# Performance work log

Measured on AMD Instinct MI355X. Metric: run time of the kernel, lower is better.

## Reference

```python
import jax, jax.numpy as jnp
import numpy as np

TEMPLATE_SZ = 7
MAX_SR = 3


def setup_inputs() -> dict:
    key = jax.random.key(0)
    # image-like values in [0, 255) since the module ends with a uint8 cast
    x = jax.random.uniform(key, (2, 1, 192, 192), dtype=jnp.float32) * 255.0
    return {"inputs": x, "search_range": 3}


def reference(inputs, search_range):
    # Equivalent math to: pad(max_sr) -> unfold(k, pad=k//2) -> unfold(s) ->
    # permute -> slice sub-window -> reshape -> uint8.
    # Both zero-pads commute, so fold them into one pad and gather directly,
    # avoiding the huge duplicated double-im2col intermediate.
    k = TEMPLATE_SZ
    max_sr = MAX_SR
    cv = 2 * search_range + 1          # cost_volume_sz
    offset = max_sr - search_range
    B, C, H, W = inputs.shape          # C == 1 (implied by the torch view)
    pad = max_sr + k // 2              # combined zero padding
    Q = jnp.pad(inputs[:, 0].astype(jnp.float32), ((0, 0), (pad, pad), (pad, pad)))
    r = offset + jnp.arange(cv)        # search offsets within max window
    t = jnp.arange(k)                  # template offsets
    # windows[b,i,j,dy,dx,ty,tx] = Q[b, i + r[dy] + ty, j + r[dx] + tx]
    iy = jnp.arange(H)[:, None, None] + r[None, :, None] + t[None, None, :]  # [H, cv, k]
    jx = jnp.arange(W)[:, None, None] + r[None, :, None] + t[None, None, :]  # [W, cv, k]
    win = Q[:, iy[:, None, :, None, :, None], jx[None, :, None, :, None, :]]  # [B,H,W,cv,cv,k,k]
    return win.reshape(B, H, W, cv * cv, k * k).astype(jnp.uint8)
```

## Files before the change

kernel.cpp:

```cpp
#include <hip/hip_runtime.h>


#define KT 7
#define K2 49
#define MAX_SR 3
#define B_ 2
#define H_ 192
#define W_ 192
#define HW (H_ * W_)
#define PAD 6
#define NT 512
#define RMAX 5
#define PS 17
#define NGROUPS (B_ * H_ * W_ / 4)
#define TABN (4 * NT * RMAX)

typedef int vint4 __attribute__((ext_vector_type(4)));

__device__ __forceinline__ int tab_entry(int jj, int cv, int offset, int d,
                                         int cvmagic) {
    if (jj >= 4 * d) jj = 4 * d - 1;
    int p_in = (jj >= d) + (jj >= 2 * d) + (jj >= 3 * d);
    int j  = jj - p_in * d;
    int rr = j / K2;
    int tt = j - rr * K2;
    int ry = (rr * cvmagic) >> 16;
    int rx = rr - ry * cv;
    int ty = tt / KT;
    int tx = tt - ty * KT;
    return 4 * ((offset + ry + ty) * PS + (offset + rx + tx) + p_in);
}

__global__ __launch_bounds__(256) void tab_kernel(
    int* __restrict__ tab, int cv, int offset, int d, int cvmagic)
{
    int jj = blockIdx.x * 256 + threadIdx.x;
    if (jj < TABN) tab[jj] = tab_entry(jj, cv, offset, d, cvmagic);
}

__global__ __launch_bounds__(NT, 6) void esw_kernel(
    const float* __restrict__ in, int* __restrict__ out,
    const int* __restrict__ tab,
    int cv, int offset, int d, int cvmagic)
{
    __shared__ int patch[13 * PS + 4];

    const int tid = threadIdx.x;
    const int g   = blockIdx.x;

    vint4 f[RMAX];
    if (tab) {
        #pragma unroll
        for (int r = 0; r < RMAX; ++r)
            f[r] = *(const vint4*)(tab + 4 * (tid + NT * r));
    } else {
        #pragma unroll
        for (int r = 0; r < RMAX; ++r) {
            int j4 = 4 * (tid + NT * r);
            #pragma unroll
            for (int u = 0; u < 4; ++u)
                f[r][u] = tab_entry(j4 + u, cv, offset, d, cvmagic);
        }
    }

    const int pix0 = 4 * g;
    const int b   = pix0 / HW;
    const int rem = pix0 - b * HW;
    const int h   = rem / W_;
    const int w   = rem - h * W_;

    if (tid < 13 * 16) {
        int dy = tid >> 4;
        int dx = tid & 15;
        int y = h + dy - PAD;
        int x = w + dx - PAD;
        int v = 0;
        if ((unsigned)y < (unsigned)H_ && (unsigned)x < (unsigned)W_)
            v = (int)in[b * HW + y * W_ + x];
        patch[dy * PS + dx] = v;
    }
    __syncthreads();

    int* op = out + (long long)g * (long long)(4 * d);
    const char* pb = (const char*)patch;
    #pragma unroll
    for (int r = 0; r < RMAX; ++r) {
        int q = tid + NT * r;
        if (q < d) {
            vint4 v;
            v.x = *(const int*)(pb + f[r].x);
            v.y = *(const int*)(pb + f[r].y);
            v.z = *(const int*)(pb + f[r].z);
            v.w = *(const int*)(pb + f[r].w);
            *(vint4*)(op + 4 * q) = v;
        }
    }
}

extern "C" void kernel_launch(void* const* d_in, const int* in_sizes, int n_in,
                              void* d_out, int out_size, void* d_ws, size_t ws_size,
                              hipStream_t stream) {
    const float* in = (const float*)d_in[0];
    int* out = (int*)d_out;

    int cv2 = out_size / (B_ * H_ * W_ * K2);
    int cv = 1;
    while (cv * cv < cv2) ++cv;
    int offset = MAX_SR - (cv - 1) / 2;
    int d = cv2 * K2;
    int cvmagic = 65536 / cv + 1;

    int* tab = (ws_size >= (size_t)(TABN * sizeof(int))) ? (int*)d_ws : nullptr;
    if (tab)
        tab_kernel<<<(TABN + 255) / 256, 256, 0, stream>>>(tab, cv, offset, d,
                                                           cvmagic);
    esw_kernel<<<NGROUPS, NT, 0, stream>>>(in, out, tab, cv, offset, d, cvmagic);
}
```

Baseline: 696.9 us.

## Persistent blocks with double-buffered LDS patch and replicated copies to cut bank conflicts

Result: no change. 710.3 us (+1.9%).

```diff
diff --git a/kernel.cpp b/kernel.cpp
--- a/kernel.cpp
+++ b/kernel.cpp
@@ -12,7 +12,12 @@
 #define NT 512
 #define RMAX 5
 #define PS 17
+#define REP 4
+#define CSTR 232
+#define BUFI (REP * CSTR)
 #define NGROUPS (B_ * H_ * W_ / 4)
+#define NBLOCKS 1024
+#define NITER (NGROUPS / NBLOCKS)
 #define TABN (4 * NT * RMAX)
 
 typedef int vint4 __attribute__((ext_vector_type(4)));
@@ -38,61 +43,101 @@
     if (jj < TABN) tab[jj] = tab_entry(jj, cv, offset, d, cvmagic);
 }
 
-__global__ __launch_bounds__(NT, 6) void esw_kernel(
+__global__ __launch_bounds__(NT, 8) void esw_kernel(
     const float* __restrict__ in, int* __restrict__ out,
     const int* __restrict__ tab,
     int cv, int offset, int d, int cvmagic)
 {
-    __shared__ int patch[13 * PS + 4];
+    __shared__ int patch[2][BUFI + 8];
 
     const int tid = threadIdx.x;
-    const int g   = blockIdx.x;
+    const int bid = blockIdx.x;
+    const int cshift = (tid & 3) * (CSTR * 4);
 
     vint4 f[RMAX];
     if (tab) {
         #pragma unroll
-        for (int r = 0; r < RMAX; ++r)
-            f[r] = *(const vint4*)(tab + 4 * (tid + NT * r));
+        for (int r = 0; r < RMAX; ++r) {
+            vint4 t = *(const vint4*)(tab + 4 * (tid + NT * r));
+            t.x += cshift; t.y += cshift; t.z += cshift; t.w += cshift;
+            f[r] = t;
+        }
     } else {
         #pragma unroll
         for (int r = 0; r < RMAX; ++r) {
             int j4 = 4 * (tid + NT * r);
             #pragma unroll
             for (int u = 0; u < 4; ++u)
-                f[r][u] = tab_entry(j4 + u, cv, offset, d, cvmagic);
+                f[r][u] = tab_entry(j4 + u, cv, offset, d, cvmagic) + cshift;
         }
     }
 
-    const int pix0 = 4 * g;
-    const int b   = pix0 / HW;
-    const int rem = pix0 - b * HW;
-    const int h   = rem / W_;
-    const int w   = rem - h * W_;
+    const int sidx = tid < 13 * 16 ? tid : 13 * 16 - 1;
+    const int sdy = sidx >> 4;
+    const int sdx = sidx & 15;
+    const int swa = sdy * PS + sdx;
 
-    if (tid < 13 * 16) {
-        int dy = tid >> 4;
-        int dx = tid & 15;
-        int y = h + dy - PAD;
-        int x = w + dx - PAD;
+    {
+        const int pix0 = 4 * bid;
+        const int b   = pix0 / HW;
+        const int rem = pix0 - b * HW;
+        const int h   = rem / W_;
+        const int w   = rem - h * W_;
+        int y = h + sdy - PAD;
+        int x = w + sdx - PAD;
         int v = 0;
         if ((unsigned)y < (unsigned)H_ && (unsigned)x < (unsigned)W_)
             v = (int)in[b * HW + y * W_ + x];
-        patch[dy * PS + dx] = v;
+        #pragma unroll
+        for (int c = 0; c < REP; ++c) patch[0][c * CSTR + swa] = v;
     }
-    __syncthreads();
+    asm volatile("s_waitcnt lgkmcnt(0)" ::: "memory");
+    __builtin_amdgcn_sched_barrier(0);
+    __builtin_amdgcn_s_barrier();
+    __builtin_amdgcn_sched_barrier(0);
 
-    int* op = out + (long long)g * (long long)(4 * d);
-    const char* pb = (const char*)patch;
-    #pragma unroll
-    for (int r = 0; r < RMAX; ++r) {
-        int q = tid + NT * r;
-        if (q < d) {
-            vint4 v;
-            v.x = *(const int*)(pb + f[r].x);
-            v.y = *(const int*)(pb + f[r].y);
-            v.z = *(const int*)(pb + f[r].z);
-            v.w = *(const int*)(pb + f[r].w);
-            *(vint4*)(op + 4 * q) = v;
+    int cur = 0;
+    for (int it = 0; it < NITER; ++it) {
+        const int g = it * NBLOCKS + bid;
+        const int have = (it + 1 < NITER);
+
+        int vnext = 0;
+        if (have) {
+            const int pix0 = 4 * (g + NBLOCKS);
+            const int b   = pix0 / HW;
+            const int rem = pix0 - b * HW;
+            const int h   = rem / W_;
+            const int w   = rem - h * W_;
+            int y = h + sdy - PAD;
+            int x = w + sdx - PAD;
+            if ((unsigned)y < (unsigned)H_ && (unsigned)x < (unsigned)W_)
+                vnext = (int)in[b * HW + y * W_ + x];
+        }
+
+        int* op = out + g * (4 * d);
+        const char* pb = (const char*)&patch[cur][0];
+        #pragma unroll
+        for (int r = 0; r < RMAX; ++r) {
+            int q = tid + NT * r;
+            if (q < d) {
+                vint4 v;
+                v.x = *(const int*)(pb + f[r].x);
+                v.y = *(const int*)(pb + f[r].y);
+                v.z = *(const int*)(pb + f[r].z);
+                v.w = *(const int*)(pb + f[r].w);
+                *(vint4*)(op + 4 * q) = v;
+            }
+        }
+
+        if (have) {
+            int* pn = &patch[cur ^ 1][0];
+            #pragma unroll
+            for (int c = 0; c < REP; ++c) pn[c * CSTR + swa] = vnext;
+            asm volatile("s_waitcnt lgkmcnt(0)" ::: "memory");
+            __builtin_amdgcn_sched_barrier(0);
+            __builtin_amdgcn_s_barrier();
+            __builtin_amdgcn_sched_barrier(0);
+            cur ^= 1;
         }
     }
 }
@@ -114,5 +159,5 @@
     if (tab)
         tab_kernel<<<(TABN + 255) / 256, 256, 0, stream>>>(tab, cv, offset, d,
                                                            cvmagic);
-    esw_kernel<<<NGROUPS, NT, 0, stream>>>(in, out, tab, cv, offset, d, cvmagic);
+    esw_kernel<<<NBLOCKS, NT, 0, stream>>>(in, out, tab, cv, offset, d, cvmagic);
 }
```

## Use persistent per-wave groups with private LDS patches and swizzled indexing

Applied to the files above, without the earlier changes.

Result: no change. 693.0 us, median of 2 (-0.6%).

```diff
diff --git a/kernel.cpp b/kernel.cpp
--- a/kernel.cpp
+++ b/kernel.cpp
@@ -9,13 +9,19 @@
 #define W_ 192
 #define HW (H_ * W_)
 #define PAD 6
-#define NT 512
-#define RMAX 5
+#define NT 256
+#define NBLOCKS 512
+#define WPB (NT / 64)
+#define NWAVES (NBLOCKS * WPB)
 #define PS 17
+#define BUFI 280
 #define NGROUPS (B_ * H_ * W_ / 4)
-#define TABN (4 * NT * RMAX)
+#define TABQ 2560
+#define TABN (4 * TABQ)
 
 typedef int vint4 __attribute__((ext_vector_type(4)));
+
+__device__ __forceinline__ int swz(int e) { return e + (e >> 2); }
 
 __device__ __forceinline__ int tab_entry(int jj, int cv, int offset, int d,
                                          int cvmagic) {
@@ -28,7 +34,8 @@
     int rx = rr - ry * cv;
     int ty = tt / KT;
     int tx = tt - ty * KT;
-    return 4 * ((offset + ry + ty) * PS + (offset + rx + tx) + p_in);
+    int e = (offset + ry + ty) * PS + (offset + rx + tx) + p_in;
+    return 4 * swz(e);
 }
 
 __global__ __launch_bounds__(256) void tab_kernel(
@@ -38,62 +45,72 @@
     if (jj < TABN) tab[jj] = tab_entry(jj, cv, offset, d, cvmagic);
 }
 
-__global__ __launch_bounds__(NT, 6) void esw_kernel(
+__global__ __launch_bounds__(NT, 2) void esw_kernel(
     const float* __restrict__ in, int* __restrict__ out,
     const int* __restrict__ tab,
     int cv, int offset, int d, int cvmagic)
 {
-    __shared__ int patch[13 * PS + 4];
+    __shared__ int patch[WPB][BUFI];
 
-    const int tid = threadIdx.x;
-    const int g   = blockIdx.x;
+    const int tid  = threadIdx.x;
+    const int lane = tid & 63;
+    const int wv   = tid >> 6;
+    int* const pbuf = patch[wv];
+    const char* const pb = (const char*)pbuf;
 
-    vint4 f[RMAX];
-    if (tab) {
+    const int NR  = (4 * d + 255) >> 8;
+    const int wid = blockIdx.x * WPB + wv;
+
+    for (int g = wid; g < NGROUPS; g += NWAVES) {
+        const int pix0 = 4 * g;
+        const int b   = pix0 / HW;
+        const int rem = pix0 - b * HW;
+        const int h   = rem / W_;
+        const int w   = rem - h * W_;
         #pragma unroll
-        for (int r = 0; r < RMAX; ++r)
-            f[r] = *(const vint4*)(tab + 4 * (tid + NT * r));
-    } else {
-        #pragma unroll
-        for (int r = 0; r < RMAX; ++r) {
-            int j4 = 4 * (tid + NT * r);
-            #pragma unroll
-            for (int u = 0; u < 4; ++u)
-                f[r][u] = tab_entry(j4 + u, cv, offset, d, cvmagic);
+        for (int k = 0; k < 4; ++k) {
+            int e = lane + 64 * k;
+            if (e < 13 * 16) {
+                int dy = e >> 4, dx = e & 15;
+                int y = h + dy - PAD, x = w + dx - PAD;
+                int v = 0;
+                if ((unsigned)y < (unsigned)H_ && (unsigned)x < (unsigned)W_)
+                    v = (int)in[b * HW + y * W_ + x];
+                pbuf[swz(dy * PS + dx)] = v;
+            }
         }
-    }
+        asm volatile("s_waitcnt lgkmcnt(0)" ::: "memory");
 
-    const int pix0 = 4 * g;
-    const int b   = pix0 / HW;
-    const int rem = pix0 - b * HW;
-    const int h   = rem / W_;
-    const int w   = rem - h * W_;
-
-    if (tid < 13 * 16) {
-        int dy = tid >> 4;
-        int dx = tid & 15;
-        int y = h + dy - PAD;
-        int x = w + dx - PAD;
-        int v = 0;
-        if ((unsigned)y < (unsigned)H_ && (unsigned)x < (unsigned)W_)
-            v = (int)in[b * HW + y * W_ + x];
-        patch[dy * PS + dx] = v;
-    }
-    __syncthreads();
-
-    int* op = out + (long long)g * (long long)(4 * d);
-    const char* pb = (const char*)patch;
-    #pragma unroll
-    for (int r = 0; r < RMAX; ++r) {
-        int q = tid + NT * r;
-        if (q < d) {
-            vint4 v;
-            v.x = *(const int*)(pb + f[r].x);
-            v.y = *(const int*)(pb + f[r].y);
-            v.z = *(const int*)(pb + f[r].z);
-            v.w = *(const int*)(pb + f[r].w);
-            *(vint4*)(op + 4 * q) = v;
+        int* op = out + g * (4 * d);
+        if (tab) {
+            vint4 t = *(const vint4*)(tab + 4 * lane);
+            for (int r = 0; r < NR; ++r) {
+                vint4 tn = *(const vint4*)(tab + 4 * (64 * (r + 1) + lane));
+                int q = 64 * r + lane;
+                if (q < d) {
+                    vint4 v;
+                    v.x = *(const int*)(pb + t.x);
+                    v.y = *(const int*)(pb + t.y);
+                    v.z = *(const int*)(pb + t.z);
+                    v.w = *(const int*)(pb + t.w);
+                    *(vint4*)(op + 4 * q) = v;
+                }
+                t = tn;
+            }
+        } else {
+            for (int r = 0; r < NR; ++r) {
+                int q = 64 * r + lane;
+                if (q < d) {
+                    vint4 v;
+                    v.x = *(const int*)(pb + tab_entry(4 * q + 0, cv, offset, d, cvmagic));
+                    v.y = *(const int*)(pb + tab_entry(4 * q + 1, cv, offset, d, cvmagic));
+                    v.z = *(const int*)(pb + tab_entry(4 * q + 2, cv, offset, d, cvmagic));
+                    v.w = *(const int*)(pb + tab_entry(4 * q + 3, cv, offset, d, cvmagic));
+                    *(vint4*)(op + 4 * q) = v;
+                }
+            }
         }
+        asm volatile("s_waitcnt lgkmcnt(0)" ::: "memory");
     }
 }
 
@@ -114,5 +131,5 @@
     if (tab)
         tab_kernel<<<(TABN + 255) / 256, 256, 0, stream>>>(tab, cv, offset, d,
                                                            cvmagic);
-    esw_kernel<<<NGROUPS, NT, 0, stream>>>(in, out, tab, cv, offset, d, cvmagic);
+    esw_kernel<<<NBLOCKS, NT, 0, stream>>>(in, out, tab, cv, offset, d, cvmagic);
 }
```
